# Kernel tuning notes

Hardware: AMD Instinct MI355X
Metric: run time of the kernel (lower is better)

## Reference

```python
import jax, jax.numpy as jnp
import numpy as np

NHID = 512
NCLS = 250
CHUNK = 200  # words per class (equal class_chunks), vocab = NCLS*CHUNK = 50000
N = 2048     # flattened tokens (batch*seq after masking)


def setup_inputs() -> dict:
    key = jax.random.key(0)
    k1, k2, k3, k4, k5 = jax.random.split(key, 5)
    r = 0.1  # init_weights uniform range
    x = jax.random.normal(k1, (N, NHID), dtype=jnp.float32)
    cls_idx = jax.random.randint(k2, (N,), 0, NCLS, dtype=jnp.int64)
    Wc = jax.random.uniform(k3, (NCLS, NHID), jnp.float32, -r, r)   # cls_decoder.weight
    bc = jnp.zeros((NCLS,), jnp.float32)                             # cls_decoder.bias
    Ww = jax.random.uniform(k4, (NCLS, CHUNK, NHID), jnp.float32, -r, r)  # stacked words_decoders weights
    bw = jnp.zeros((NCLS, CHUNK), jnp.float32)                       # stacked words_decoders biases
    return {"x": x, "Wc": Wc, "bc": bc, "Ww": Ww, "bw": bw, "cls_idx": cls_idx}


def reference(x, Wc, bc, Ww, bw, cls_idx):
    # Class logits for every token: cls_decoder(input)
    p_class = jnp.einsum('nh,ch->nc', x, Wc) + bc          # [N, NCLS]
    # Per-class word decoders: each token goes through the Linear of its class.
    # Equivalent to the dict-based index_select + per-class Linear in the
    # original forward (rows reordered per-token instead of grouped by class).
    Wg = Ww[cls_idx]                                       # [N, CHUNK, NHID] irregular gather
    bg = bw[cls_idx]                                       # [N, CHUNK]
    p_words = jnp.einsum('nkh,nh->nk', Wg, x) + bg         # [N, CHUNK]
    # Concatenate class and within-class logits into one array output.
    return jnp.concatenate([p_class, p_words], axis=1)     # [N, NCLS+CHUNK]
```

## Files before the change

### kernel.cpp

```cpp
#include <hip/hip_runtime.h>

#define NHID   512
#define NCLS   250
#define CHUNK  200
#define NTOK   2048
#define NOUT   450
#define NTHR   128
#define NBLK   258
#define MAXTOK 32

typedef __attribute__((ext_vector_type(8))) short bf16x8;
typedef __attribute__((ext_vector_type(4))) float f32x4;

#define MFMA(a, b, c) __builtin_amdgcn_mfma_f32_16x16x32_bf16((a), (b), (c), 0, 0, 0)

__device__ __forceinline__ unsigned hpack(unsigned a, unsigned b) {
    return __builtin_amdgcn_perm(a, b, 0x07060302u);
}

__device__ __forceinline__ void cvt8(float4 va, float4 vb, bf16x8& h, bf16x8& l) {
    unsigned u0 = __float_as_uint(va.x), u1 = __float_as_uint(va.y);
    unsigned u2 = __float_as_uint(va.z), u3 = __float_as_uint(va.w);
    unsigned u4 = __float_as_uint(vb.x), u5 = __float_as_uint(vb.y);
    unsigned u6 = __float_as_uint(vb.z), u7 = __float_as_uint(vb.w);
    union { unsigned w[4]; bf16x8 v; } H, L;
    H.w[0] = hpack(u1, u0); H.w[1] = hpack(u3, u2);
    H.w[2] = hpack(u5, u4); H.w[3] = hpack(u7, u6);
    float r0 = va.x - __uint_as_float(u0 & 0xffff0000u);
    float r1 = va.y - __uint_as_float(u1 & 0xffff0000u);
    float r2 = va.z - __uint_as_float(u2 & 0xffff0000u);
    float r3 = va.w - __uint_as_float(u3 & 0xffff0000u);
    float r4 = vb.x - __uint_as_float(u4 & 0xffff0000u);
    float r5 = vb.y - __uint_as_float(u5 & 0xffff0000u);
    float r6 = vb.z - __uint_as_float(u6 & 0xffff0000u);
    float r7 = vb.w - __uint_as_float(u7 & 0xffff0000u);
    L.w[0] = hpack(__float_as_uint(r1), __float_as_uint(r0));
    L.w[1] = hpack(__float_as_uint(r3), __float_as_uint(r2));
    L.w[2] = hpack(__float_as_uint(r5), __float_as_uint(r4));
    L.w[3] = hpack(__float_as_uint(r7), __float_as_uint(r6));
    h = H.v; l = L.v;
}

__device__ __forceinline__ void async16(const float* g, float* lds_base) {
    __builtin_amdgcn_global_load_lds(
        (const __attribute__((address_space(1))) unsigned*)g,
        (__attribute__((address_space(3))) unsigned*)lds_base, 16, 0, 0);
}

__device__ __forceinline__ void lds_fence_wave() {
    __builtin_amdgcn_wave_barrier();
    asm volatile("s_waitcnt lgkmcnt(0)" ::: "memory");
    __builtin_amdgcn_wave_barrier();
}

__global__ __launch_bounds__(NTHR, 1)
void cbd_fused(const float* __restrict__ x,  const float* __restrict__ Wc,
               const float* __restrict__ bc, const float* __restrict__ Ww,
               const float* __restrict__ bw, const int* __restrict__ cls_idx,
               float* __restrict__ out)
{
    __shared__ short Afrag[2][16 * 64 * 8];
    __shared__ float Bbuf[2][16 * 256];

    const int bid  = blockIdx.x;
    const int tid  = threadIdx.x;
    const int wid  = tid >> 6;
    const int lane = tid & 63;
    const int n    = lane & 15;
    const int q    = lane >> 4;

    if (wid == 1) {
        if (bid < 256) {
            const int mt = bid >> 1, hn = bid & 1;
            const float* ap = x + (size_t)(mt * 16 + n) * NHID + q * 8;
            #pragma unroll
            for (int g4 = 0; g4 < 2; ++g4) {
                const float* bp[4]; float bias[4]; int col[4]; bool rv[4];
                #pragma unroll
                for (int k = 0; k < 4; ++k) {
                    int r = (hn * 8 + g4 * 4 + k) * 16 + n;
                    rv[k] = r < NCLS;
                    int rc = rv[k] ? r : NCLS - 1;
                    bp[k]   = Wc + (size_t)rc * NHID + q * 8;
                    bias[k] = bc[rc];
                    col[k]  = rc;
                }
                f32x4 acc[4] = {{0,0,0,0},{0,0,0,0},{0,0,0,0},{0,0,0,0}};
                #pragma unroll 2
                for (int s = 0; s < 16; ++s) {
                    float4 a0 = *(const float4*)(ap + s * 32);
                    float4 a1 = *(const float4*)(ap + s * 32 + 4);
                    bf16x8 ah, al; cvt8(a0, a1, ah, al);
                    #pragma unroll
                    for (int k = 0; k < 4; ++k) {
                        float4 b0 = *(const float4*)(bp[k] + s * 32);
                        float4 b1 = *(const float4*)(bp[k] + s * 32 + 4);
                        bf16x8 bh, bl; cvt8(b0, b1, bh, bl);
                        acc[k] = MFMA(ah, bh, acc[k]);
                        acc[k] = MFMA(al, bh, acc[k]);
                        acc[k] = MFMA(ah, bl, acc[k]);
                    }
                }
                #pragma unroll
                for (int k = 0; k < 4; ++k)
                    if (rv[k]) {
                        #pragma unroll
                        for (int i = 0; i < 4; ++i)
                            out[(size_t)(mt * 16 + q * 4 + i) * NOUT + col[k]]
                                = acc[k][i] + bias[k];
                    }
            }
        }
        return;
    }

    int myvals[32];
    #pragma unroll
    for (int it = 0; it < 8; ++it) {
        int4 v = *(const int4*)&cls_idx[it * 256 + lane * 4];
        myvals[it*4+0] = v.x; myvals[it*4+1] = v.y;
        myvals[it*4+2] = v.z; myvals[it*4+3] = v.w;
    }

    int c, slotbase;
    const float* wsrc;
    bool issued01 = false;
    if (bid < NCLS) {
        c = bid; slotbase = 0;
        wsrc = Ww + (size_t)c * CHUNK * NHID;
        #pragma unroll
        for (int r = 0; r < 16; ++r)
            async16(wsrc + (size_t)r * NHID + lane * 4, &Bbuf[0][r * 256]);
        #pragma unroll
        for (int r = 0; r < 16; ++r)
            async16(wsrc + (size_t)r * NHID + 256 + lane * 4, &Bbuf[1][r * 256]);
        issued01 = true;
    } else {
        int* hist = (int*)&Bbuf[0][0];
        for (int i = lane; i < 256; i += 64) hist[i] = 0;
        lds_fence_wave();
        #pragma unroll
        for (int j = 0; j < 32; ++j) atomicAdd(&hist[myvals[j]], 1);
        lds_fence_wave();
        int kk = bid - NCLS, found = -1, runbase = 0;
        #pragma unroll
        for (int ch = 0; ch < 4; ++ch) {
            int hv = hist[ch * 64 + lane];
            unsigned long long m = __ballot(hv > 16);
            int c2 = (int)__popcll(m);
            if (found < 0 && kk < runbase + c2) {
                unsigned long long mm = m;
                for (int t = 0; t < 8; ++t) if (t < kk - runbase) mm &= mm - 1;
                found = ch * 64 + (__ffsll((long long)mm) - 1);
            }
            runbase += c2;
        }
        if (found < 0) return;
        c = found; slotbase = 16;
        wsrc = Ww + (size_t)c * CHUNK * NHID;
    }

    int* toktmp = (int*)&Afrag[0][0];
    int cnt = 0;
    #pragma unroll
    for (int j = 0; j < 32; ++j) {
        int idx  = (j >> 2) * 256 + lane * 4 + (j & 3);
        bool hit = (myvals[j] == c);
        unsigned long long m = __ballot(hit);
        if (hit) {
            int pos = cnt + (int)__popcll(m & ((1ull << lane) - 1ull));
            if (pos < MAXTOK) toktmp[pos] = idx;
        }
        cnt += (int)__popcll(m);
    }
    const int cntc = cnt < MAXTOK ? cnt : MAXTOK;
    if (slotbase >= cntc || cntc == 0) {
        if (issued01) asm volatile("s_waitcnt vmcnt(0)" ::: "memory");
        return;
    }
    lds_fence_wave();
    int idx_slot = slotbase + n;
    int mytokr   = toktmp[idx_slot < cntc ? idx_slot : 0];
    lds_fence_wave();

    if (!issued01) {
        #pragma unroll
        for (int r = 0; r < 16; ++r)
            async16(wsrc + (size_t)r * NHID + lane * 4, &Bbuf[0][r * 256]);
        #pragma unroll
        for (int r = 0; r < 16; ++r)
            async16(wsrc + (size_t)r * NHID + 256 + lane * 4, &Bbuf[1][r * 256]);
    }

    int tkS[4]; bool msk[4];
    #pragma unroll
    for (int i = 0; i < 4; ++i) {
        int ml = q * 4 + i;
        tkS[i] = __shfl(mytokr, ml);
        msk[i] = (slotbase + ml) < cntc;
    }

    {
        int tk = __shfl(mytokr, n);
        #pragma unroll
        for (int it = 0; it < 16; ++it) {
            const float* xp = x + (size_t)tk * NHID + it * 32 + q * 8;
            float4 va = *(const float4*)xp, vb = *(const float4*)(xp + 4);
            bf16x8 hh, ll; cvt8(va, vb, hh, ll);
            int u = it * 64 + lane;
            *(bf16x8*)&Afrag[0][u * 8] = hh;
            *(bf16x8*)&Afrag[1][u * 8] = ll;
        }
    }
    lds_fence_wave();

    f32x4 acc = {0.f, 0.f, 0.f, 0.f};
    for (int hp = 0; hp < 26; ++hp) {
        const int p = hp >> 1, h = hp & 1, buf = hp & 1;
        asm volatile("s_waitcnt vmcnt(0)" ::: "memory");
        __builtin_amdgcn_wave_barrier();

        if (h == 0) { acc[0] = 0.f; acc[1] = 0.f; acc[2] = 0.f; acc[3] = 0.f; }
        #pragma unroll
        for (int ss = 0; ss < 8; ++ss) {
            const int sg = h * 8 + ss;
            bf16x8 ah = *(const bf16x8*)&Afrag[0][(sg * 64 + lane) * 8];
            bf16x8 al = *(const bf16x8*)&Afrag[1][(sg * 64 + lane) * 8];
            const float* bq = &Bbuf[buf][n * 256 + ss * 32 + q * 8];
            float4 b0 = *(const float4*)bq;
            float4 b1 = *(const float4*)(bq + 4);
            bf16x8 bh, bl; cvt8(b0, b1, bh, bl);
            acc = MFMA(ah, bh, acc);
            acc = MFMA(al, bh, acc);
            acc = MFMA(ah, bl, acc);
        }

        if (h == 1) {
            int r = p * 16 + n;
            if (r < CHUNK) {
                float bias = bw[c * CHUNK + r];
                #pragma unroll
                for (int i = 0; i < 4; ++i)
                    if (msk[i])
                        out[(size_t)tkS[i] * NOUT + NCLS + r] = acc[i] + bias;
            }
        }

        if (hp + 2 < 26) {
            const int p2 = (hp + 2) >> 1, h2 = (hp + 2) & 1;
            const int nrow = (p2 == 12) ? 8 : 16;
            const float* base = wsrc + (size_t)(p2 * 16) * NHID + h2 * 256 + lane * 4;
            for (int r = 0; r < nrow; ++r)
                async16(base + (size_t)r * NHID, &Bbuf[buf][r * 256]);
        }
    }
}

extern "C" void kernel_launch(void* const* d_in, const int* in_sizes, int n_in,
                              void* d_out, int out_size, void* d_ws, size_t ws_size,
                              hipStream_t stream) {
    const float* x   = (const float*)d_in[0];
    const float* Wc  = (const float*)d_in[1];
    const float* bc  = (const float*)d_in[2];
    const float* Ww  = (const float*)d_in[3];
    const float* bw  = (const float*)d_in[4];
    const int*   cls = (const int*)d_in[5];
    float* out = (float*)d_out;
    hipLaunchKernelGGL(cbd_fused, dim3(NBLK), dim3(NTHR), 0, stream,
                       x, Wc, bc, Ww, bw, cls, out);
}
```

Baseline: 190.6 us.

## Deepen weight prefetch pipeline with partial vmcnt waits and padded LDS rows

Replaces the full vmcnt(0) drain each step with vmcnt(16), so the next half-tile's async weight loads stay in flight while the current one is consumed. The last tile always issues 16 clamped rows so the wait count stays fixed. LDS rows are padded to 260 floats to reduce bank conflicts on the B reads. The first weight loads are issued early for every block, including overflow blocks, and biases are staged in shared memory. This costs a few redundant loads and extra LDS, and relies on exact vmcnt accounting for correctness.

```diff
diff --git a/kernel.cpp b/kernel.cpp
--- a/kernel.cpp
+++ b/kernel.cpp
@@ -8,6 +8,7 @@
 #define NTHR   128
 #define NBLK   258
 #define MAXTOK 32
+#define BPAD   260
 
 typedef __attribute__((ext_vector_type(8))) short bf16x8;
 typedef __attribute__((ext_vector_type(4))) float f32x4;
@@ -60,7 +61,8 @@
                float* __restrict__ out)
 {
     __shared__ short Afrag[2][16 * 64 * 8];
-    __shared__ float Bbuf[2][16 * 256];
+    __shared__ float Bbuf[2][16 * BPAD];
+    __shared__ float bias_s[208];
 
     const int bid  = blockIdx.x;
     const int tid  = threadIdx.x;
@@ -123,20 +125,10 @@
     }
 
     int c, slotbase;
-    const float* wsrc;
-    bool issued01 = false;
     if (bid < NCLS) {
         c = bid; slotbase = 0;
-        wsrc = Ww + (size_t)c * CHUNK * NHID;
-        #pragma unroll
-        for (int r = 0; r < 16; ++r)
-            async16(wsrc + (size_t)r * NHID + lane * 4, &Bbuf[0][r * 256]);
-        #pragma unroll
-        for (int r = 0; r < 16; ++r)
-            async16(wsrc + (size_t)r * NHID + 256 + lane * 4, &Bbuf[1][r * 256]);
-        issued01 = true;
     } else {
-        int* hist = (int*)&Bbuf[0][0];
+        int* hist = (int*)&Afrag[1][0];
         for (int i = lane; i < 256; i += 64) hist[i] = 0;
         lds_fence_wave();
         #pragma unroll
@@ -155,10 +147,18 @@
             }
             runbase += c2;
         }
+        lds_fence_wave();
         if (found < 0) return;
         c = found; slotbase = 16;
-        wsrc = Ww + (size_t)c * CHUNK * NHID;
-    }
+    }
+    const float* wsrc = Ww + (size_t)c * CHUNK * NHID;
+
+    #pragma unroll
+    for (int r = 0; r < 16; ++r)
+        async16(wsrc + (size_t)r * NHID + lane * 4, &Bbuf[0][r * BPAD]);
+    #pragma unroll
+    for (int r = 0; r < 16; ++r)
+        async16(wsrc + (size_t)r * NHID + 256 + lane * 4, &Bbuf[1][r * BPAD]);
 
     int* toktmp = (int*)&Afrag[0][0];
     int cnt = 0;
@@ -174,8 +174,8 @@
         cnt += (int)__popcll(m);
     }
     const int cntc = cnt < MAXTOK ? cnt : MAXTOK;
-    if (slotbase >= cntc || cntc == 0) {
-        if (issued01) asm volatile("s_waitcnt vmcnt(0)" ::: "memory");
+    if (slotbase >= cntc) {
+        asm volatile("s_waitcnt vmcnt(0)" ::: "memory");
         return;
     }
     lds_fence_wave();
@@ -183,15 +183,6 @@
     int mytokr   = toktmp[idx_slot < cntc ? idx_slot : 0];
     lds_fence_wave();
 
-    if (!issued01) {
-        #pragma unroll
-        for (int r = 0; r < 16; ++r)
-            async16(wsrc + (size_t)r * NHID + lane * 4, &Bbuf[0][r * 256]);
-        #pragma unroll
-        for (int r = 0; r < 16; ++r)
-            async16(wsrc + (size_t)r * NHID + 256 + lane * 4, &Bbuf[1][r * 256]);
-    }
-
     int tkS[4]; bool msk[4];
     #pragma unroll
     for (int i = 0; i < 4; ++i) {
@@ -199,6 +190,8 @@
         tkS[i] = __shfl(mytokr, ml);
         msk[i] = (slotbase + ml) < cntc;
     }
+
+    for (int i = lane; i < CHUNK; i += 64) bias_s[i] = bw[c * CHUNK + i];
 
     {
         int tk = __shfl(mytokr, n);
@@ -216,17 +209,17 @@
 
     f32x4 acc = {0.f, 0.f, 0.f, 0.f};
     for (int hp = 0; hp < 26; ++hp) {
+        if (hp < 25) asm volatile("s_waitcnt vmcnt(16)" ::: "memory");
+        else         asm volatile("s_waitcnt vmcnt(0)"  ::: "memory");
+
         const int p = hp >> 1, h = hp & 1, buf = hp & 1;
-        asm volatile("s_waitcnt vmcnt(0)" ::: "memory");
-        __builtin_amdgcn_wave_barrier();
-
         if (h == 0) { acc[0] = 0.f; acc[1] = 0.f; acc[2] = 0.f; acc[3] = 0.f; }
         #pragma unroll
         for (int ss = 0; ss < 8; ++ss) {
             const int sg = h * 8 + ss;
             bf16x8 ah = *(const bf16x8*)&Afrag[0][(sg * 64 + lane) * 8];
             bf16x8 al = *(const bf16x8*)&Afrag[1][(sg * 64 + lane) * 8];
-            const float* bq = &Bbuf[buf][n * 256 + ss * 32 + q * 8];
+            const float* bq = &Bbuf[buf][n * BPAD + ss * 32 + q * 8];
             float4 b0 = *(const float4*)bq;
             float4 b1 = *(const float4*)(bq + 4);
             bf16x8 bh, bl; cvt8(b0, b1, bh, bl);
@@ -238,7 +231,7 @@
         if (h == 1) {
             int r = p * 16 + n;
             if (r < CHUNK) {
-                float bias = bw[c * CHUNK + r];
+                float bias = bias_s[r];
                 #pragma unroll
                 for (int i = 0; i < 4; ++i)
                     if (msk[i])
@@ -248,10 +241,13 @@
 
         if (hp + 2 < 26) {
             const int p2 = (hp + 2) >> 1, h2 = (hp + 2) & 1;
-            const int nrow = (p2 == 12) ? 8 : 16;
-            const float* base = wsrc + (size_t)(p2 * 16) * NHID + h2 * 256 + lane * 4;
-            for (int r = 0; r < nrow; ++r)
-                async16(base + (size_t)r * NHID, &Bbuf[buf][r * 256]);
+            const int koff = h2 * 256;
+            #pragma unroll
+            for (int r = 0; r < 16; ++r) {
+                int rr = p2 * 16 + r; if (rr > CHUNK - 1) rr = CHUNK - 1;
+                async16(wsrc + (size_t)rr * NHID + koff + lane * 4,
+                        &Bbuf[buf][r * BPAD]);
+            }
         }
     }
 }
```

Measured after the change: 179.9 us. 5.6% less time.
